# Kernel optimization log

Hardware: AMD Instinct MI355X
Metric: run time of the kernel (lower is better)

The kernel has to match this reference:

```python
import jax, jax.numpy as jnp
import numpy as np

N, E, F_IN, H, G, C = 50000, 800000, 128, 128, 64, 10
EPS = 1e-5


def _glorot_lin(key, fin, fout):
    s = 1.0 / np.sqrt(fin)
    return jax.random.uniform(key, (fin, fout), jnp.float32, -s, s)


def setup_inputs() -> dict:
    key = jax.random.key(0)
    ks = jax.random.split(key, 24)
    x = jax.random.normal(ks[0], (N, F_IN), jnp.float32)
    edge_index = jax.random.randint(ks[1], (2, E), 0, N)
    batch = jnp.sort(jax.random.randint(ks[2], (N,), 0, G))
    inp = {"x": x, "edge_index": edge_index, "batch": batch}
    # GCNConv weights [in, out] and biases
    dims = [(F_IN, H), (H, H), (H, H), (H, H)]
    for i, (fi, fo) in enumerate(dims, start=1):
        inp[f"W{i}"] = _glorot_lin(ks[2 + i], fi, fo)
        inp[f"b{i}"] = jnp.zeros((fo,), jnp.float32)
    # BatchNorm affine params
    for i in range(1, 4):
        inp[f"g{i}"] = jnp.ones((H,), jnp.float32)
        inp[f"be{i}"] = jnp.zeros((H,), jnp.float32)
    # MLP head
    inp["lw1"] = _glorot_lin(ks[10], 2 * H, H)
    inp["lb1"] = jnp.zeros((H,), jnp.float32)
    inp["lw2"] = _glorot_lin(ks[11], H, C)
    inp["lb2"] = jnp.zeros((C,), jnp.float32)
    return inp


def _gcn_conv(h_in, W, b, src, dst, norm_e, self_norm):
    # linear transform then symmetric-normalized aggregation (incl. self loops)
    h = h_in @ W                                            # [N, out]
    agg = jax.ops.segment_sum(h[src] * norm_e[:, None], dst, num_segments=N)
    return agg + h * self_norm[:, None] + b


def _batch_norm(x, gamma, beta):
    mu = jnp.mean(x, axis=0)
    var = jnp.var(x, axis=0)
    return (x - mu) * jax.lax.rsqrt(var + EPS) * gamma + beta


def reference(x, edge_index, batch, W1, b1, W2, b2, W3, b3, W4, b4,
              g1, be1, g2, be2, g3, be3, lw1, lb1, lw2, lb2):
    src, dst = edge_index[0], edge_index[1]
    # degrees with self loops; GCN symmetric normalization
    deg = jax.ops.segment_sum(jnp.ones((E,), jnp.float32), dst, num_segments=N) + 1.0
    dinv = jax.lax.rsqrt(deg)
    norm_e = dinv[src] * dinv[dst]   # per-edge norm
    self_norm = 1.0 / deg            # self-loop norm = dinv*dinv

    h = jax.nn.relu(_batch_norm(_gcn_conv(x, W1, b1, src, dst, norm_e, self_norm), g1, be1))
    h = jax.nn.relu(_batch_norm(_gcn_conv(h, W2, b2, src, dst, norm_e, self_norm), g2, be2))
    h = jax.nn.relu(_batch_norm(_gcn_conv(h, W3, b3, src, dst, norm_e, self_norm), g3, be3))
    h = jax.nn.relu(_gcn_conv(h, W4, b4, src, dst, norm_e, self_norm))

    counts = jax.ops.segment_sum(jnp.ones((N,), jnp.float32), batch, num_segments=G)
    x_mean = jax.ops.segment_sum(h, batch, num_segments=G) / counts[:, None]
    x_max = jax.ops.segment_max(h, batch, num_segments=G)
    z = jnp.concatenate([x_mean, x_max], axis=1)            # [G, 2H]

    z = jax.nn.relu(z @ lw1 + lb1)
    # dropout is identity in eval mode
    return z @ lw2 + lb2                                    # [G, C]
```

## Files before the change

### kernel.cpp

```cpp
#include <hip/hip_runtime.h>

#define N_NODES 50000
#define N_EDGES 800000
#define HID     128
#define NGRAPH  64
#define BN_EPS  1e-5f
#define SCAN_B  98
#define AGG_GRID 2048

__global__ __launch_bounds__(256) void degbounds_kernel(const int* __restrict__ ei,
                                                        int* __restrict__ degi,
                                                        const int* __restrict__ batch,
                                                        int* __restrict__ bound) {
    const int i = blockIdx.x * 256 + threadIdx.x;
    if (i < N_EDGES) atomicAdd(&degi[ei[N_EDGES + i]], 1);
    if (i < N_NODES) {
        const int b = batch[i];
        if (i == 0) {
            for (int g = 0; g <= b; ++g) bound[g] = 0;
        } else {
            const int pb = batch[i - 1];
            for (int g = pb + 1; g <= b; ++g) bound[g] = i;
        }
        if (i == N_NODES - 1) {
            for (int g = b + 1; g <= NGRAPH; ++g) bound[g] = N_NODES;
        }
    }
}

__global__ __launch_bounds__(512) void scan1_kernel(const int* __restrict__ degi,
                                                    int* __restrict__ row_start,
                                                    int* __restrict__ partials,
                                                    float* __restrict__ dinv) {
    __shared__ int sh[512];
    const int t = threadIdx.x;
    const int i = blockIdx.x * 512 + t;
    const int v = (i < N_NODES) ? degi[i] : 0;
    if (i < N_NODES) dinv[i] = rsqrtf((float)v + 1.0f);
    sh[t] = v;
    __syncthreads();
#pragma unroll
    for (int off = 1; off < 512; off <<= 1) {
        const int add = (t >= off) ? sh[t - off] : 0;
        __syncthreads();
        sh[t] += add;
        __syncthreads();
    }
    if (i < N_NODES) row_start[i] = sh[t] - v;
    if (t == 511) partials[blockIdx.x] = sh[511];
}

__global__ __launch_bounds__(128) void scan2_kernel(int* __restrict__ partials,
                                                    int* __restrict__ row_start) {
    __shared__ int sh[SCAN_B + 1];
    const int t = threadIdx.x;
    if (t < SCAN_B) sh[t] = partials[t];
    __syncthreads();
    if (t == 0) {
        int run = 0;
        for (int b = 0; b < SCAN_B; ++b) { const int v = sh[b]; sh[b] = run; run += v; }
        sh[SCAN_B] = run;
    }
    __syncthreads();
    if (t < SCAN_B) partials[t] = sh[t];
    if (t == 0) row_start[N_NODES] = sh[SCAN_B];
}

__global__ __launch_bounds__(512) void scan3_kernel(int* __restrict__ row_start,
                                                    const int* __restrict__ partials) {
    const int i = blockIdx.x * 512 + threadIdx.x;
    if (i < N_NODES) row_start[i] += partials[blockIdx.x];
}

__global__ __launch_bounds__(256) void scatter_kernel(const int* __restrict__ ei,
                                                      const float* __restrict__ dinv,
                                                      const int* __restrict__ row_start,
                                                      int* __restrict__ cursor,
                                                      float2* __restrict__ csr_sw) {
    int e = blockIdx.x * 256 + threadIdx.x;
    if (e >= N_EDGES) return;
    const int src = ei[e];
    const int dst = ei[N_EDGES + e];
    const int pos = row_start[dst] + atomicAdd(&cursor[dst], 1);
    float2 sw;
    sw.x = __int_as_float(src);
    sw.y = dinv[src] * dinv[dst];
    csr_sw[pos] = sw;
}

__global__ __launch_bounds__(256) void gemm_kernel(const float* __restrict__ X,
                                                   const float* __restrict__ W,
                                                   const float* __restrict__ stats,
                                                   const float* __restrict__ gamma,
                                                   const float* __restrict__ beta,
                                                   const int use_bn,
                                                   float* __restrict__ hout) {
    __shared__ float xs[64][128];
    __shared__ float wsm[32][128];
    __shared__ float scs[128], shs[128];
    const int tid = threadIdx.x;
    const int block_row = blockIdx.x * 64;

    if (use_bn && tid < 128) {
        const float invN = 1.0f / (float)N_NODES;
        const float mu = stats[tid] * invN;
        const float var = stats[128 + tid] * invN - mu * mu;
        const float sc = rsqrtf(var + BN_EPS) * gamma[tid];
        scs[tid] = sc;
        shs[tid] = fmaf(-mu, sc, beta[tid]);
    }
    if (use_bn) __syncthreads();

    {
        int rows_valid = N_NODES - block_row;
        if (rows_valid > 64) rows_valid = 64;
        for (int i = tid; i < 64 * 32; i += 256) {
            const int r = i >> 5;
            const int c4 = (i & 31) * 4;
            float4 v = make_float4(0.f, 0.f, 0.f, 0.f);
            if (r < rows_valid)
                v = *(const float4*)(X + (size_t)(block_row + r) * HID + c4);
            if (use_bn) {
                const float4 sc = *(const float4*)&scs[c4];
                const float4 sh = *(const float4*)&shs[c4];
                v.x = fmaxf(fmaf(v.x, sc.x, sh.x), 0.f);
                v.y = fmaxf(fmaf(v.y, sc.y, sh.y), 0.f);
                v.z = fmaxf(fmaf(v.z, sc.z, sh.z), 0.f);
                v.w = fmaxf(fmaf(v.w, sc.w, sh.w), 0.f);
            }
            *(float4*)&xs[r][c4 ^ (((r >> 2) & 3) << 2)] = v;
        }
    }

    const int cgA = (tid & 15) * 4;
    const int r0 = (tid >> 4) * 4;
    const int kswz = ((r0 >> 2) & 3) << 2;

    float acc[4][8];
#pragma unroll
    for (int r = 0; r < 4; ++r)
#pragma unroll
        for (int j = 0; j < 8; ++j) acc[r][j] = 0.f;

    for (int kc = 0; kc < 4; ++kc) {
        __syncthreads();
        {
            const float4* Wv = (const float4*)(W + kc * 32 * HID);
            float4* wsv = (float4*)&wsm[0][0];
            for (int i = tid; i < 32 * 32; i += 256) wsv[i] = Wv[i];
        }
        __syncthreads();
#pragma unroll
        for (int kk4 = 0; kk4 < 32; kk4 += 4) {
            float4 xv[4];
#pragma unroll
            for (int j = 0; j < 4; ++j)
                xv[j] = *(const float4*)&xs[r0 + j][(kc * 32 + kk4) ^ kswz];
#pragma unroll
            for (int dk = 0; dk < 4; ++dk) {
                const float4 wa = *(const float4*)&wsm[kk4 + dk][cgA];
                const float4 wb = *(const float4*)&wsm[kk4 + dk][cgA + 64];
#pragma unroll
                for (int r = 0; r < 4; ++r) {
                    const float xvv = ((const float*)&xv[r])[dk];
                    acc[r][0] = fmaf(xvv, wa.x, acc[r][0]);
                    acc[r][1] = fmaf(xvv, wa.y, acc[r][1]);
                    acc[r][2] = fmaf(xvv, wa.z, acc[r][2]);
                    acc[r][3] = fmaf(xvv, wa.w, acc[r][3]);
                    acc[r][4] = fmaf(xvv, wb.x, acc[r][4]);
                    acc[r][5] = fmaf(xvv, wb.y, acc[r][5]);
                    acc[r][6] = fmaf(xvv, wb.z, acc[r][6]);
                    acc[r][7] = fmaf(xvv, wb.w, acc[r][7]);
                }
            }
        }
    }

#pragma unroll
    for (int r = 0; r < 4; ++r) {
        const int row = block_row + r0 + r;
        if (row < N_NODES) {
            float* hp = hout + (size_t)row * HID;
            *(float4*)(hp + cgA) =
                make_float4(acc[r][0], acc[r][1], acc[r][2], acc[r][3]);
            *(float4*)(hp + cgA + 64) =
                make_float4(acc[r][4], acc[r][5], acc[r][6], acc[r][7]);
        }
    }
}

__global__ __launch_bounds__(256) void agg_csr_kernel(const int* __restrict__ row_start,
                                                      const float2* __restrict__ csr_sw,
                                                      const float* __restrict__ h,
                                                      const float* __restrict__ dinv,
                                                      const float* __restrict__ bias,
                                                      float* __restrict__ agg,
                                                      float* __restrict__ stats_out,
                                                      const int do_stats) {
    const int lane = threadIdx.x & 63;
    const int wv = threadIdx.x >> 6;
    const int c = lane * 2;
    const float2 bv = *(const float2*)(bias + c);

    float2 ssum = make_float2(0.f, 0.f);
    float2 ssq  = make_float2(0.f, 0.f);

    for (int base = blockIdx.x * 4; base < N_NODES; base += AGG_GRID * 4) {
        const int node = base + wv;
        if (node >= N_NODES) continue;
        const int beg = row_start[node];
        const int end = row_start[node + 1];

        const float dv = dinv[node];
        const float sn = dv * dv;
        const float2 hv = *(const float2*)(h + (size_t)node * HID + c);
        float2 a0 = make_float2(fmaf(hv.x, sn, bv.x), fmaf(hv.y, sn, bv.y));
        float2 a1 = make_float2(0.f, 0.f), a2 = make_float2(0.f, 0.f),
               a3 = make_float2(0.f, 0.f), a4 = make_float2(0.f, 0.f),
               a5 = make_float2(0.f, 0.f), a6 = make_float2(0.f, 0.f),
               a7 = make_float2(0.f, 0.f);

        int p = beg;
        for (; p + 8 <= end; p += 8) {
            const float2 e0 = csr_sw[p];
            const float2 e1 = csr_sw[p + 1];
            const float2 e2 = csr_sw[p + 2];
            const float2 e3 = csr_sw[p + 3];
            const float2 e4 = csr_sw[p + 4];
            const float2 e5 = csr_sw[p + 5];
            const float2 e6 = csr_sw[p + 6];
            const float2 e7 = csr_sw[p + 7];
            const float2 v0 = *(const float2*)(h + (size_t)__float_as_int(e0.x) * HID + c);
            const float2 v1 = *(const float2*)(h + (size_t)__float_as_int(e1.x) * HID + c);
            const float2 v2 = *(const float2*)(h + (size_t)__float_as_int(e2.x) * HID + c);
            const float2 v3 = *(const float2*)(h + (size_t)__float_as_int(e3.x) * HID + c);
            const float2 v4 = *(const float2*)(h + (size_t)__float_as_int(e4.x) * HID + c);
            const float2 v5 = *(const float2*)(h + (size_t)__float_as_int(e5.x) * HID + c);
            const float2 v6 = *(const float2*)(h + (size_t)__float_as_int(e6.x) * HID + c);
            const float2 v7 = *(const float2*)(h + (size_t)__float_as_int(e7.x) * HID + c);
            a0.x = fmaf(v0.x, e0.y, a0.x); a0.y = fmaf(v0.y, e0.y, a0.y);
            a1.x = fmaf(v1.x, e1.y, a1.x); a1.y = fmaf(v1.y, e1.y, a1.y);
            a2.x = fmaf(v2.x, e2.y, a2.x); a2.y = fmaf(v2.y, e2.y, a2.y);
            a3.x = fmaf(v3.x, e3.y, a3.x); a3.y = fmaf(v3.y, e3.y, a3.y);
            a4.x = fmaf(v4.x, e4.y, a4.x); a4.y = fmaf(v4.y, e4.y, a4.y);
            a5.x = fmaf(v5.x, e5.y, a5.x); a5.y = fmaf(v5.y, e5.y, a5.y);
            a6.x = fmaf(v6.x, e6.y, a6.x); a6.y = fmaf(v6.y, e6.y, a6.y);
            a7.x = fmaf(v7.x, e7.y, a7.x); a7.y = fmaf(v7.y, e7.y, a7.y);
        }
        for (; p + 4 <= end; p += 4) {
            const float2 e0 = csr_sw[p];
            const float2 e1 = csr_sw[p + 1];
            const float2 e2 = csr_sw[p + 2];
            const float2 e3 = csr_sw[p + 3];
            const float2 v0 = *(const float2*)(h + (size_t)__float_as_int(e0.x) * HID + c);
            const float2 v1 = *(const float2*)(h + (size_t)__float_as_int(e1.x) * HID + c);
            const float2 v2 = *(const float2*)(h + (size_t)__float_as_int(e2.x) * HID + c);
            const float2 v3 = *(const float2*)(h + (size_t)__float_as_int(e3.x) * HID + c);
            a0.x = fmaf(v0.x, e0.y, a0.x); a0.y = fmaf(v0.y, e0.y, a0.y);
            a1.x = fmaf(v1.x, e1.y, a1.x); a1.y = fmaf(v1.y, e1.y, a1.y);
            a2.x = fmaf(v2.x, e2.y, a2.x); a2.y = fmaf(v2.y, e2.y, a2.y);
            a3.x = fmaf(v3.x, e3.y, a3.x); a3.y = fmaf(v3.y, e3.y, a3.y);
        }
        for (; p < end; ++p) {
            const float2 e0 = csr_sw[p];
            const float2 v0 = *(const float2*)(h + (size_t)__float_as_int(e0.x) * HID + c);
            a0.x = fmaf(v0.x, e0.y, a0.x); a0.y = fmaf(v0.y, e0.y, a0.y);
        }
        a0.x += (a1.x + a2.x) + (a3.x + a4.x) + (a5.x + a6.x) + a7.x;
        a0.y += (a1.y + a2.y) + (a3.y + a4.y) + (a5.y + a6.y) + a7.y;
        *(float2*)(agg + (size_t)node * HID + c) = a0;

        ssum.x += a0.x; ssum.y += a0.y;
        ssq.x = fmaf(a0.x, a0.x, ssq.x); ssq.y = fmaf(a0.y, a0.y, ssq.y);
    }

    if (do_stats) {
        __shared__ float s1[4][128];
        __shared__ float s2[4][128];
        s1[wv][c] = ssum.x; s1[wv][c + 1] = ssum.y;
        s2[wv][c] = ssq.x;  s2[wv][c + 1] = ssq.y;
        __syncthreads();
        const int t = threadIdx.x;
        if (t < 128) {
            atomicAdd(&stats_out[t], s1[0][t] + s1[1][t] + s1[2][t] + s1[3][t]);
        } else {
            const int c2 = t - 128;
            atomicAdd(&stats_out[128 + c2], s2[0][c2] + s2[1][c2] + s2[2][c2] + s2[3][c2]);
        }
    }
}

__global__ __launch_bounds__(256) void pool_seg_kernel(const float* __restrict__ a,
                                                       const int* __restrict__ bound,
                                                       float* __restrict__ z) {
    const int g = blockIdx.x;
    const int cl = threadIdx.x & 31;
    const int c = blockIdx.y * 32 + cl;
    const int par = threadIdx.x >> 5;
    const int beg = bound[g], end = bound[g + 1];
    float s = 0.f, m = 0.f;
    for (int r = beg + par; r < end; r += 8) {
        const float v = fmaxf(a[(size_t)r * HID + c], 0.f);
        s += v;
        m = fmaxf(m, v);
    }
    __shared__ float ssum[8][32];
    __shared__ float smax[8][32];
    ssum[par][cl] = s;
    smax[par][cl] = m;
    __syncthreads();
    if (par == 0) {
        float ts = 0.f, tm = 0.f;
#pragma unroll
        for (int p = 0; p < 8; ++p) { ts += ssum[p][cl]; tm = fmaxf(tm, smax[p][cl]); }
        const float cntf = (float)(end - beg);
        z[g * 256 + c] = ts / fmaxf(cntf, 1.f);
        z[g * 256 + 128 + c] = tm;
    }
}

__global__ __launch_bounds__(128) void head_kernel(const float* __restrict__ z,
                                                   const float* __restrict__ lw1,
                                                   const float* __restrict__ lb1,
                                                   const float* __restrict__ lw2,
                                                   const float* __restrict__ lb2,
                                                   float* __restrict__ out) {
    __shared__ float zin[256];
    __shared__ float z1[128];
    const int g = blockIdx.x;
    const int t = threadIdx.x;
    zin[t] = z[g * 256 + t];
    zin[128 + t] = z[g * 256 + 128 + t];
    __syncthreads();
    float accv = lb1[t];
#pragma unroll 4
    for (int k = 0; k < 256; ++k) accv = fmaf(zin[k], lw1[k * 128 + t], accv);
    z1[t] = fmaxf(accv, 0.f);
    __syncthreads();
    if (t < 10) {
        float o = lb2[t];
#pragma unroll 4
        for (int k = 0; k < 128; ++k) o = fmaf(z1[k], lw2[k * 10 + t], o);
        out[g * 10 + t] = o;
    }
}

extern "C" void kernel_launch(void* const* d_in, const int* in_sizes, int n_in,
                              void* d_out, int out_size, void* d_ws, size_t ws_size,
                              hipStream_t stream) {
    const float* x     = (const float*)d_in[0];
    const int*   ei    = (const int*)d_in[1];
    const int*   batch = (const int*)d_in[2];
    const float* W[4]  = {(const float*)d_in[3], (const float*)d_in[5],
                          (const float*)d_in[7], (const float*)d_in[9]};
    const float* B[4]  = {(const float*)d_in[4], (const float*)d_in[6],
                          (const float*)d_in[8], (const float*)d_in[10]};
    const float* Gm[3] = {(const float*)d_in[11], (const float*)d_in[13],
                          (const float*)d_in[15]};
    const float* Be[3] = {(const float*)d_in[12], (const float*)d_in[14],
                          (const float*)d_in[16]};
    const float* lw1 = (const float*)d_in[17];
    const float* lb1 = (const float*)d_in[18];
    const float* lw2 = (const float*)d_in[19];
    const float* lb2 = (const float*)d_in[20];

    char* ws = (char*)d_ws;
    float*  dinv      = (float*)ws;
    float*  stats3    = (float*)(ws + 50000u * 4);
    float*  z         = (float*)(ws + 50768u * 4);
    int*    degi      = (int*)  (ws + 67152u * 4);
    int*    cursor    = (int*)  (ws + 117152u * 4);
    int*    row_start = (int*)  (ws + 167152u * 4);
    int*    bound     = (int*)  (ws + 217156u * 4);
    float2* csr_sw    = (float2*)(ws + 217224u * 4);
    float*  hbuf      = (float*)(ws + 1817224u * 4);
    float*  abuf      = (float*)(ws + 8217224u * 4);
    int*    partials  = (int*)  (ws + 14617224u * 4);

    hipMemsetAsync(degi, 0, 100000u * sizeof(int), stream);
    hipMemsetAsync(stats3, 0, 768u * sizeof(float), stream);
    degbounds_kernel<<<(N_EDGES + 255) / 256, 256, 0, stream>>>(ei, degi, batch, bound);
    scan1_kernel<<<SCAN_B, 512, 0, stream>>>(degi, row_start, partials, dinv);
    scan2_kernel<<<1, 128, 0, stream>>>(partials, row_start);
    scan3_kernel<<<SCAN_B, 512, 0, stream>>>(row_start, partials);
    scatter_kernel<<<(N_EDGES + 255) / 256, 256, 0, stream>>>(ei, dinv, row_start,
                                                              cursor, csr_sw);

    const float* cur = x;
    for (int l = 0; l < 4; ++l) {
        gemm_kernel<<<(N_NODES + 63) / 64, 256, 0, stream>>>(
            cur, W[l], l > 0 ? stats3 + (l - 1) * 256 : stats3,
            l > 0 ? Gm[l - 1] : Gm[0], l > 0 ? Be[l - 1] : Be[0],
            l > 0 ? 1 : 0, hbuf);
        agg_csr_kernel<<<AGG_GRID, 256, 0, stream>>>(
            row_start, csr_sw, hbuf, dinv, B[l], abuf,
            l < 3 ? stats3 + l * 256 : stats3, l < 3 ? 1 : 0);
        cur = abuf;
    }

    pool_seg_kernel<<<dim3(NGRAPH, 4), 256, 0, stream>>>(abuf, bound, z);
    head_kernel<<<NGRAPH, 128, 0, stream>>>(z, lw1, lb1, lw2, lb2, (float*)d_out);
}
```

Baseline: 756.4 us.

## Unfuse BN statistics from aggregation and launch one wave per node

The aggregation kernel no longer walks nodes in a grid-stride loop with a fixed grid. It now launches one block per four nodes, each wave handling a single node, and its per-block BatchNorm sum and sum-of-squares reduction is removed. A separate bn_stats_kernel rereads the aggregated output to compute those column statistics with atomics. This gives a simpler, fully parallel gather kernel, at the cost of an extra launch and an extra full read of the N×128 activations for each of the first three layers.

After: 741.9 us. No clear change (-1.9%).

```diff
diff --git a/kernel.cpp b/kernel.cpp
--- a/kernel.cpp
+++ b/kernel.cpp
@@ -6,7 +6,6 @@
 #define NGRAPH  64
 #define BN_EPS  1e-5f
 #define SCAN_B  98
-#define AGG_GRID 2048
 
 __global__ __launch_bounds__(256) void degbounds_kernel(const int* __restrict__ ei,
                                                         int* __restrict__ degi,
@@ -194,99 +193,95 @@
                                                       const float* __restrict__ h,
                                                       const float* __restrict__ dinv,
                                                       const float* __restrict__ bias,
-                                                      float* __restrict__ agg,
-                                                      float* __restrict__ stats_out,
-                                                      const int do_stats) {
+                                                      float* __restrict__ agg) {
+    const int node = blockIdx.x * 4 + (threadIdx.x >> 6);
+    if (node >= N_NODES) return;
     const int lane = threadIdx.x & 63;
-    const int wv = threadIdx.x >> 6;
     const int c = lane * 2;
+    const int beg = row_start[node];
+    const int end = row_start[node + 1];
+
+    const float dv = dinv[node];
+    const float sn = dv * dv;
+    const float2 hv = *(const float2*)(h + (size_t)node * HID + c);
     const float2 bv = *(const float2*)(bias + c);
-
-    float2 ssum = make_float2(0.f, 0.f);
-    float2 ssq  = make_float2(0.f, 0.f);
-
-    for (int base = blockIdx.x * 4; base < N_NODES; base += AGG_GRID * 4) {
-        const int node = base + wv;
-        if (node >= N_NODES) continue;
-        const int beg = row_start[node];
-        const int end = row_start[node + 1];
-
-        const float dv = dinv[node];
-        const float sn = dv * dv;
-        const float2 hv = *(const float2*)(h + (size_t)node * HID + c);
-        float2 a0 = make_float2(fmaf(hv.x, sn, bv.x), fmaf(hv.y, sn, bv.y));
-        float2 a1 = make_float2(0.f, 0.f), a2 = make_float2(0.f, 0.f),
-               a3 = make_float2(0.f, 0.f), a4 = make_float2(0.f, 0.f),
-               a5 = make_float2(0.f, 0.f), a6 = make_float2(0.f, 0.f),
-               a7 = make_float2(0.f, 0.f);
-
-        int p = beg;
-        for (; p + 8 <= end; p += 8) {
-            const float2 e0 = csr_sw[p];
-            const float2 e1 = csr_sw[p + 1];
-            const float2 e2 = csr_sw[p + 2];
-            const float2 e3 = csr_sw[p + 3];
-            const float2 e4 = csr_sw[p + 4];
-            const float2 e5 = csr_sw[p + 5];
-            const float2 e6 = csr_sw[p + 6];
-            const float2 e7 = csr_sw[p + 7];
-            const float2 v0 = *(const float2*)(h + (size_t)__float_as_int(e0.x) * HID + c);
-            const float2 v1 = *(const float2*)(h + (size_t)__float_as_int(e1.x) * HID + c);
-            const float2 v2 = *(const float2*)(h + (size_t)__float_as_int(e2.x) * HID + c);
-            const float2 v3 = *(const float2*)(h + (size_t)__float_as_int(e3.x) * HID + c);
-            const float2 v4 = *(const float2*)(h + (size_t)__float_as_int(e4.x) * HID + c);
-            const float2 v5 = *(const float2*)(h + (size_t)__float_as_int(e5.x) * HID + c);
-            const float2 v6 = *(const float2*)(h + (size_t)__float_as_int(e6.x) * HID + c);
-            const float2 v7 = *(const float2*)(h + (size_t)__float_as_int(e7.x) * HID + c);
-            a0.x = fmaf(v0.x, e0.y, a0.x); a0.y = fmaf(v0.y, e0.y, a0.y);
-            a1.x = fmaf(v1.x, e1.y, a1.x); a1.y = fmaf(v1.y, e1.y, a1.y);
-            a2.x = fmaf(v2.x, e2.y, a2.x); a2.y = fmaf(v2.y, e2.y, a2.y);
-            a3.x = fmaf(v3.x, e3.y, a3.x); a3.y = fmaf(v3.y, e3.y, a3.y);
-            a4.x = fmaf(v4.x, e4.y, a4.x); a4.y = fmaf(v4.y, e4.y, a4.y);
-            a5.x = fmaf(v5.x, e5.y, a5.x); a5.y = fmaf(v5.y, e5.y, a5.y);
-            a6.x = fmaf(v6.x, e6.y, a6.x); a6.y = fmaf(v6.y, e6.y, a6.y);
-            a7.x = fmaf(v7.x, e7.y, a7.x); a7.y = fmaf(v7.y, e7.y, a7.y);
-        }
-        for (; p + 4 <= end; p += 4) {
-            const float2 e0 = csr_sw[p];
-            const float2 e1 = csr_sw[p + 1];
-            const float2 e2 = csr_sw[p + 2];
-            const float2 e3 = csr_sw[p + 3];
-            const float2 v0 = *(const float2*)(h + (size_t)__float_as_int(e0.x) * HID + c);
-            const float2 v1 = *(const float2*)(h + (size_t)__float_as_int(e1.x) * HID + c);
-            const float2 v2 = *(const float2*)(h + (size_t)__float_as_int(e2.x) * HID + c);
-            const float2 v3 = *(const float2*)(h + (size_t)__float_as_int(e3.x) * HID + c);
-            a0.x = fmaf(v0.x, e0.y, a0.x); a0.y = fmaf(v0.y, e0.y, a0.y);
-            a1.x = fmaf(v1.x, e1.y, a1.x); a1.y = fmaf(v1.y, e1.y, a1.y);
-            a2.x = fmaf(v2.x, e2.y, a2.x); a2.y = fmaf(v2.y, e2.y, a2.y);
-            a3.x = fmaf(v3.x, e3.y, a3.x); a3.y = fmaf(v3.y, e3.y, a3.y);
-        }
-        for (; p < end; ++p) {
-            const float2 e0 = csr_sw[p];
-            const float2 v0 = *(const float2*)(h + (size_t)__float_as_int(e0.x) * HID + c);
-            a0.x = fmaf(v0.x, e0.y, a0.x); a0.y = fmaf(v0.y, e0.y, a0.y);
-        }
-        a0.x += (a1.x + a2.x) + (a3.x + a4.x) + (a5.x + a6.x) + a7.x;
-        a0.y += (a1.y + a2.y) + (a3.y + a4.y) + (a5.y + a6.y) + a7.y;
-        *(float2*)(agg + (size_t)node * HID + c) = a0;
-
-        ssum.x += a0.x; ssum.y += a0.y;
-        ssq.x = fmaf(a0.x, a0.x, ssq.x); ssq.y = fmaf(a0.y, a0.y, ssq.y);
-    }
-
-    if (do_stats) {
-        __shared__ float s1[4][128];
-        __shared__ float s2[4][128];
-        s1[wv][c] = ssum.x; s1[wv][c + 1] = ssum.y;
-        s2[wv][c] = ssq.x;  s2[wv][c + 1] = ssq.y;
-        __syncthreads();
-        const int t = threadIdx.x;
-        if (t < 128) {
-            atomicAdd(&stats_out[t], s1[0][t] + s1[1][t] + s1[2][t] + s1[3][t]);
-        } else {
-            const int c2 = t - 128;
-            atomicAdd(&stats_out[128 + c2], s2[0][c2] + s2[1][c2] + s2[2][c2] + s2[3][c2]);
-        }
+    float2 a0 = make_float2(fmaf(hv.x, sn, bv.x), fmaf(hv.y, sn, bv.y));
+    float2 a1 = make_float2(0.f, 0.f), a2 = make_float2(0.f, 0.f),
+           a3 = make_float2(0.f, 0.f), a4 = make_float2(0.f, 0.f),
+           a5 = make_float2(0.f, 0.f), a6 = make_float2(0.f, 0.f),
+           a7 = make_float2(0.f, 0.f);
+
+    int p = beg;
+    for (; p + 8 <= end; p += 8) {
+        const float2 e0 = csr_sw[p];
+        const float2 e1 = csr_sw[p + 1];
+        const float2 e2 = csr_sw[p + 2];
+        const float2 e3 = csr_sw[p + 3];
+        const float2 e4 = csr_sw[p + 4];
+        const float2 e5 = csr_sw[p + 5];
+        const float2 e6 = csr_sw[p + 6];
+        const float2 e7 = csr_sw[p + 7];
+        const float2 v0 = *(const float2*)(h + (size_t)__float_as_int(e0.x) * HID + c);
+        const float2 v1 = *(const float2*)(h + (size_t)__float_as_int(e1.x) * HID + c);
+        const float2 v2 = *(const float2*)(h + (size_t)__float_as_int(e2.x) * HID + c);
+        const float2 v3 = *(const float2*)(h + (size_t)__float_as_int(e3.x) * HID + c);
+        const float2 v4 = *(const float2*)(h + (size_t)__float_as_int(e4.x) * HID + c);
+        const float2 v5 = *(const float2*)(h + (size_t)__float_as_int(e5.x) * HID + c);
+        const float2 v6 = *(const float2*)(h + (size_t)__float_as_int(e6.x) * HID + c);
+        const float2 v7 = *(const float2*)(h + (size_t)__float_as_int(e7.x) * HID + c);
+        a0.x = fmaf(v0.x, e0.y, a0.x); a0.y = fmaf(v0.y, e0.y, a0.y);
+        a1.x = fmaf(v1.x, e1.y, a1.x); a1.y = fmaf(v1.y, e1.y, a1.y);
+        a2.x = fmaf(v2.x, e2.y, a2.x); a2.y = fmaf(v2.y, e2.y, a2.y);
+        a3.x = fmaf(v3.x, e3.y, a3.x); a3.y = fmaf(v3.y, e3.y, a3.y);
+        a4.x = fmaf(v4.x, e4.y, a4.x); a4.y = fmaf(v4.y, e4.y, a4.y);
+        a5.x = fmaf(v5.x, e5.y, a5.x); a5.y = fmaf(v5.y, e5.y, a5.y);
+        a6.x = fmaf(v6.x, e6.y, a6.x); a6.y = fmaf(v6.y, e6.y, a6.y);
+        a7.x = fmaf(v7.x, e7.y, a7.x); a7.y = fmaf(v7.y, e7.y, a7.y);
+    }
+    for (; p + 4 <= end; p += 4) {
+        const float2 e0 = csr_sw[p];
+        const float2 e1 = csr_sw[p + 1];
+        const float2 e2 = csr_sw[p + 2];
+        const float2 e3 = csr_sw[p + 3];
+        const float2 v0 = *(const float2*)(h + (size_t)__float_as_int(e0.x) * HID + c);
+        const float2 v1 = *(const float2*)(h + (size_t)__float_as_int(e1.x) * HID + c);
+        const float2 v2 = *(const float2*)(h + (size_t)__float_as_int(e2.x) * HID + c);
+        const float2 v3 = *(const float2*)(h + (size_t)__float_as_int(e3.x) * HID + c);
+        a0.x = fmaf(v0.x, e0.y, a0.x); a0.y = fmaf(v0.y, e0.y, a0.y);
+        a1.x = fmaf(v1.x, e1.y, a1.x); a1.y = fmaf(v1.y, e1.y, a1.y);
+        a2.x = fmaf(v2.x, e2.y, a2.x); a2.y = fmaf(v2.y, e2.y, a2.y);
+        a3.x = fmaf(v3.x, e3.y, a3.x); a3.y = fmaf(v3.y, e3.y, a3.y);
+    }
+    for (; p < end; ++p) {
+        const float2 e0 = csr_sw[p];
+        const float2 v0 = *(const float2*)(h + (size_t)__float_as_int(e0.x) * HID + c);
+        a0.x = fmaf(v0.x, e0.y, a0.x); a0.y = fmaf(v0.y, e0.y, a0.y);
+    }
+    a0.x += (a1.x + a2.x) + (a3.x + a4.x) + (a5.x + a6.x) + a7.x;
+    a0.y += (a1.y + a2.y) + (a3.y + a4.y) + (a5.y + a6.y) + a7.y;
+    *(float2*)(agg + (size_t)node * HID + c) = a0;
+}
+
+__global__ __launch_bounds__(256) void bn_stats_kernel(const float* __restrict__ a,
+                                                       float* __restrict__ stats) {
+    const int c = threadIdx.x & 127;
+    const int half = threadIdx.x >> 7;
+    const int row0 = blockIdx.x * 128;
+    int rend = row0 + 128;
+    if (rend > N_NODES) rend = N_NODES;
+    float s = 0.f, sq = 0.f;
+    for (int r = row0 + half; r < rend; r += 2) {
+        const float v = a[(size_t)r * HID + c];
+        s += v;
+        sq = fmaf(v, v, sq);
+    }
+    __shared__ float sh[2][2][128];
+    sh[0][half][c] = s;
+    sh[1][half][c] = sq;
+    __syncthreads();
+    if (half == 0) {
+        atomicAdd(&stats[c], sh[0][0][c] + sh[0][1][c]);
+        atomicAdd(&stats[HID + c], sh[1][0][c] + sh[1][1][c]);
     }
 }
 
@@ -392,9 +387,11 @@
             cur, W[l], l > 0 ? stats3 + (l - 1) * 256 : stats3,
             l > 0 ? Gm[l - 1] : Gm[0], l > 0 ? Be[l - 1] : Be[0],
             l > 0 ? 1 : 0, hbuf);
-        agg_csr_kernel<<<AGG_GRID, 256, 0, stream>>>(
-            row_start, csr_sw, hbuf, dinv, B[l], abuf,
-            l < 3 ? stats3 + l * 256 : stats3, l < 3 ? 1 : 0);
+        agg_csr_kernel<<<(N_NODES + 3) / 4, 256, 0, stream>>>(row_start, csr_sw, hbuf,
+                                                              dinv, B[l], abuf);
+        if (l < 3)
+            bn_stats_kernel<<<(N_NODES + 127) / 128, 256, 0, stream>>>(
+                abuf, stats3 + l * 256);
         cur = abuf;
     }
 
```
